# Optimization experiments

Hardware: AMD Instinct MI355X
Metric: run time of the kernel (lower is better)

The kernel has to match this reference:

```python
import jax, jax.numpy as jnp
import numpy as np

N_NODES = 6144
IN_FEATURES = 256
N_HEADS = 4
N_HIDDEN = 64  # out_features, concat=False
LEAKY_SLOPE = 0.2
NEG_INF = -9e16


def setup_inputs() -> dict:
    key = jax.random.key(0)
    k1, k2, k3, k4 = jax.random.split(key, 4)
    h = jax.random.normal(k1, (N_NODES, IN_FEATURES), dtype=jnp.float32)
    adj_mat = jax.random.randint(k2, (N_NODES, N_NODES), 0, 2, dtype=jnp.int32)
    W = jax.random.normal(k3, (IN_FEATURES, N_HEADS * N_HIDDEN), dtype=jnp.float32) * 0.06
    a = jax.random.normal(k4, (N_HEADS, 2 * N_HIDDEN, 1), dtype=jnp.float32) * 0.1
    return {"h": h, "adj_mat": adj_mat, "W": W, "a": a}


def reference(h, adj_mat, W, a):
    n_nodes = h.shape[0]
    # linear transform, dropout is identity in eval mode
    ht = (h @ W).reshape(n_nodes, N_HEADS, N_HIDDEN).transpose(1, 0, 2)  # [H, N, d]
    a_src = a[:, :N_HIDDEN, 0]   # [H, d]
    a_tgt = a[:, N_HIDDEN:, 0]   # [H, d]
    src = jnp.einsum('hnd,hd->hn', ht, a_src)  # [H, N]
    tgt = jnp.einsum('hnd,hd->hn', ht, a_tgt)  # [H, N]
    e = src[:, :, None] + tgt[:, None, :]       # [H, N, N]
    e = jnp.where(e >= 0, e, LEAKY_SLOPE * e)    # leaky relu
    e = jnp.where(adj_mat[None, :, :] > 0, e, jnp.float32(NEG_INF))
    attention = jax.nn.softmax(e, axis=-1)       # [H, N, N]
    h_prime = jnp.einsum('hij,hjd->hid', attention, ht)  # [H, N, d]
    return h_prime.mean(axis=0)                  # [N, d] (concat=False)
```

## Files before the change

kernel.cpp:

```cpp
#include <hip/hip_runtime.h>
#include <hip/hip_bf16.h>

#define N_NODES 6144
#define IN_F 256
#define N_HEADS 4
#define N_HID 64
#define JS 8
#define JLEN (N_NODES / JS)
#define NW (JLEN / 32)
#define SM_STRIDE 25
#define PACK_BLOCKS 768
#define ACC_F32 (N_HEADS * N_NODES * N_HID + N_HEADS * N_NODES)
#define ZERO_F4_PER_BLOCK 520

typedef __attribute__((ext_vector_type(4))) float floatx4;
typedef _Float16 half2_t __attribute__((ext_vector_type(2)));
typedef _Float16 half8_t __attribute__((ext_vector_type(8)));
typedef __attribute__((ext_vector_type(4))) unsigned uint4_t;
typedef short short2v __attribute__((ext_vector_type(2)));

__device__ __forceinline__ void atomAddF32(float* p, float v) {
    unsafeAtomicAdd(p, v);
}

__global__ __launch_bounds__(256) void prep_kernel(
    const float* __restrict__ h, const float* __restrict__ W,
    const float* __restrict__ a, const int* __restrict__ adj,
    short* __restrict__ htF, float* __restrict__ srcv,
    unsigned* __restrict__ tE1pk, unsigned* __restrict__ tE2pk,
    unsigned long long* __restrict__ gmask, float* __restrict__ accZero)
{
    __shared__ float As[32][34];
    __shared__ float Bs[32][68];
    __shared__ float redS[32][16];
    __shared__ float redT[32][16];
    __shared__ unsigned short eh1[32], eh2[32];

    if (blockIdx.x < PACK_BLOCKS) {
        {
            float4* z = (float4*)accZero + (size_t)blockIdx.x * ZERO_F4_PER_BLOCK;
            const float4 zv = {0.f, 0.f, 0.f, 0.f};
            for (int i = threadIdx.x; i < ZERO_F4_PER_BLOCK; i += 256) z[i] = zv;
        }
        const int lane = threadIdx.x & 63;
        const int wave = threadIdx.x >> 6;
        const int wbase = (blockIdx.x * 4 + wave) * 192;
        for (int k0 = 0; k0 < 192; k0 += 16) {
            int v[16];
            #pragma unroll
            for (int s = 0; s < 16; ++s) {
                const int widx = wbase + k0 + s;
                const int r = widx / 96, c = widx % 96;
                v[s] = adj[(size_t)r * N_NODES + c * 64 + lane];
            }
            #pragma unroll
            for (int s = 0; s < 16; ++s) {
                const unsigned long long b = __ballot(v[s] > 0);
                const int widx = wbase + k0 + s;
                const int r = widx / 96, c = widx % 96;
                const int jcp = c / 12, wl = c % 12;
                if (lane == 0)
                    gmask[((size_t)jcp * N_NODES + r) * 12 + wl] = b;
            }
        }
        return;
    }

    const int gbx = blockIdx.x - PACK_BLOCKS;
    const int head = gbx & 3;
    const int i0 = (gbx >> 2) * 32;
    const int tid = threadIdx.x;
    const int tx = tid & 15, ty = tid >> 4;

    float acc[2][4] = {};

    for (int k0 = 0; k0 < IN_F; k0 += 32) {
        __syncthreads();
        {
            const int m = tid >> 3, kq = tid & 7;
            const float4 v = *(const float4*)(h + (i0 + m) * IN_F + k0 + kq * 4);
            As[kq*4+0][m] = v.x; As[kq*4+1][m] = v.y;
            As[kq*4+2][m] = v.z; As[kq*4+3][m] = v.w;
        }
        #pragma unroll
        for (int it = 0; it < 2; ++it) {
            int l = it * 256 + tid;
            int k = l >> 4, nq = l & 15;
            *(float4*)&Bs[k][nq*4] = *(const float4*)(W + (k0 + k) * 256 + head * 64 + nq * 4);
        }
        __syncthreads();
        #pragma unroll
        for (int kk = 0; kk < 32; ++kk) {
            const float2 av = *(const float2*)&As[kk][ty*2];
            const float4 bv = *(const float4*)&Bs[kk][tx*4];
            const float aa[2] = {av.x, av.y};
            const float bb[4] = {bv.x, bv.y, bv.z, bv.w};
            #pragma unroll
            for (int r = 0; r < 2; ++r)
                #pragma unroll
                for (int c = 0; c < 4; ++c)
                    acc[r][c] = fmaf(aa[r], bb[c], acc[r][c]);
        }
    }

    #pragma unroll
    for (int r = 0; r < 2; ++r)
        #pragma unroll
        for (int c2 = 0; c2 < 4; ++c2) {
            const int d = tx * 4 + c2;
            const int j = i0 + ty * 2 + r;
            const int jt = j >> 5, q = (j >> 3) & 3, u = j & 7;
            const int c = d >> 4, n = d & 15;
            const size_t F = (((((size_t)head * 192 + jt) * 4 + c) * 16 + n) * 4 + q) * 8 + u;
            const _Float16 hv = (_Float16)acc[r][c2];
            htF[F] = *(const short*)&hv;
        }

    float as_[4], at_[4];
    #pragma unroll
    for (int c = 0; c < 4; ++c) {
        as_[c] = a[head * 128 + tx * 4 + c];
        at_[c] = a[head * 128 + 64 + tx * 4 + c];
    }
    #pragma unroll
    for (int r = 0; r < 2; ++r) {
        float ps = 0.f, pt = 0.f;
        #pragma unroll
        for (int c = 0; c < 4; ++c) {
            ps = fmaf(acc[r][c], as_[c], ps);
            pt = fmaf(acc[r][c], at_[c], pt);
        }
        redS[ty*2+r][tx] = ps;
        redT[ty*2+r][tx] = pt;
    }
    __syncthreads();
    if (tid < 64) {
        const int row = tid & 31;
        const float* src = (tid < 32) ? &redS[row][0] : &redT[row][0];
        float s = 0.f;
        #pragma unroll
        for (int x = 0; x < 16; ++x) s += src[x];
        if (tid < 32) {
            srcv[head * N_NODES + i0 + row] = s;
        } else {
            const _Float16 E1 = (_Float16)__expf(s);
            const _Float16 E2 = (_Float16)__expf(0.2f * s);
            eh1[row] = *(const unsigned short*)&E1;
            eh2[row] = *(const unsigned short*)&E2;
        }
    }
    __syncthreads();
    if (tid < 16) {
        const unsigned v1 = (unsigned)eh1[2*tid] | ((unsigned)eh1[2*tid+1] << 16);
        const unsigned v2 = (unsigned)eh2[2*tid] | ((unsigned)eh2[2*tid+1] << 16);
        tE1pk[head * (N_NODES/2) + i0/2 + tid] = v1;
        tE2pk[head * (N_NODES/2) + i0/2 + tid] = v2;
    }
}

__global__ __launch_bounds__(256, 4) void gat_main_kernel(
    const unsigned* __restrict__ gmask32, const short* __restrict__ htF,
    const float* __restrict__ srcv, const unsigned* __restrict__ tE1pk,
    const unsigned* __restrict__ tE2pk,
    float* __restrict__ accNg, float* __restrict__ accDg)
{
    __shared__ unsigned smask[32 * SM_STRIDE];

    const int bid = blockIdx.x;
    const int xcd = bid & 7;
    const int idx = bid >> 3;
    const int jc = idx / 24;
    const int rb0 = ((idx % 24) * 8 + xcd) * 32;

    const int lane = threadIdx.x;
    const int head = threadIdx.y;
    const int m = lane & 15, quad = lane >> 4;
    const int jbase = jc * JLEN;
    const int tid = head * 64 + lane;

    {
        const unsigned* g = gmask32 + ((size_t)jc * N_NODES + rb0) * 24;
        #pragma unroll
        for (int it = 0; it < 3; ++it) {
            const int f = it * 256 + tid;
            smask[(f / 24) * SM_STRIDE + (f % 24)] = g[f];
        }
    }
    __syncthreads();

    half2_t e1s[2], e2s[2];
    #pragma unroll
    for (int t = 0; t < 2; ++t) {
        const float sv = srcv[head * N_NODES + rb0 + t * 16 + m];
        const _Float16 a1 = (_Float16)__expf(sv);
        const _Float16 a2 = (_Float16)__expf(0.2f * sv);
        e1s[t] = (half2_t){a1, a1};
        e2s[t] = (half2_t){a2, a2};
    }

    const short* fb = htF + ((size_t)(head * 192 + (jbase >> 5)) * 4) * 512 + (m * 4 + quad) * 8;
    const unsigned* pe1 = tE1pk + head * (N_NODES/2) + (jbase >> 1) + quad * 4;
    const unsigned* pe2 = tE2pk + head * (N_NODES/2) + (jbase >> 1) + quad * 4;

    half8_t bones;
    #pragma unroll
    for (int u = 0; u < 8; ++u) bones[u] = (_Float16)1.0f;

    floatx4 accN[2][4];
    floatx4 accD[2];
    #pragma unroll
    for (int t = 0; t < 2; ++t) {
        accD[t] = (floatx4){0,0,0,0};
        #pragma unroll
        for (int c = 0; c < 4; ++c) accN[t][c] = (floatx4){0,0,0,0};
    }

    half8_t bn[4];
    #pragma unroll
    for (int c = 0; c < 4; ++c) bn[c] = *(const half8_t*)(fb + c * 512);
    uint4_t E1n = *(const uint4_t*)pe1;
    uint4_t E2n = *(const uint4_t*)pe2;

    for (int w = 0; w < NW; ++w) {
        half8_t bc[4];
        #pragma unroll
        for (int c = 0; c < 4; ++c) bc[c] = bn[c];
        const uint4_t E1 = E1n, E2 = E2n;

        const int wn = (w + 1 < NW) ? (w + 1) : w;
        #pragma unroll
        for (int c = 0; c < 4; ++c)
            bn[c] = *(const half8_t*)(fb + (size_t)wn * 2048 + c * 512);
        E1n = *(const uint4_t*)(pe1 + wn * 16);
        E2n = *(const uint4_t*)(pe2 + wn * 16);

        const unsigned E1a[4] = {E1.x, E1.y, E1.z, E1.w};
        const unsigned E2a[4] = {E2.x, E2.y, E2.z, E2.w};

        #pragma unroll
        for (int t = 0; t < 2; ++t) {
            const unsigned bits = (smask[(t * 16 + m) * SM_STRIDE + w] >> (quad * 8)) & 0xffu;
            const short2v tt = __builtin_bit_cast(short2v, bits * 0x10001u);
            uint4_t af_u;
            #pragma unroll
            for (int p = 0; p < 4; ++p) {
                const short2v shl = (p == 0) ? (short2v){15,14} : (p == 1) ? (short2v){13,12}
                                 : (p == 2) ? (short2v){11,10} : (short2v){9,8};
                const short2v k = (tt << shl) >> (short2v){15,15};
                const half2_t p1 = __builtin_bit_cast(half2_t, E1a[p]) * e1s[t];
                const half2_t p2 = __builtin_bit_cast(half2_t, E2a[p]) * e2s[t];
                const half2_t mx = __builtin_elementwise_max(p1, p2);
                const unsigned r = __builtin_bit_cast(unsigned, mx) & __builtin_bit_cast(unsigned, k);
                if (p == 0) af_u.x = r; else if (p == 1) af_u.y = r;
                else if (p == 2) af_u.z = r; else af_u.w = r;
            }
            const half8_t af = __builtin_bit_cast(half8_t, af_u);
            #pragma unroll
            for (int c = 0; c < 4; ++c)
                accN[t][c] = __builtin_amdgcn_mfma_f32_16x16x32_f16(af, bc[c], accN[t][c], 0, 0, 0);
            accD[t] = __builtin_amdgcn_mfma_f32_16x16x32_f16(af, bones, accD[t], 0, 0, 0);
        }
    }

    const size_t nb = (size_t)head * N_NODES;
    #pragma unroll
    for (int t = 0; t < 2; ++t) {
        #pragma unroll
        for (int r = 0; r < 4; ++r) {
            const int gi = rb0 + t * 16 + quad * 4 + r;
            if (m == 0) atomAddF32(&accDg[nb + gi], accD[t][r]);
            float* np_ = accNg + (nb + gi) * N_HID + m;
            atomAddF32(np_ + 0,  accN[t][0][r]);
            atomAddF32(np_ + 16, accN[t][1][r]);
            atomAddF32(np_ + 32, accN[t][2][r]);
            atomAddF32(np_ + 48, accN[t][3][r]);
        }
    }
}

__global__ __launch_bounds__(256) void finalize_kernel(
    const float* __restrict__ accNg, const float* __restrict__ accDg,
    float* __restrict__ out)
{
    const int idx = blockIdx.x * 256 + threadIdx.x;
    if (idx >= N_NODES * 16) return;
    const int i = idx >> 4;
    const int d4 = (idx & 15) * 4;
    float sx = 0.f, sy = 0.f, sz = 0.f, sw = 0.f;
    #pragma unroll
    for (int hh = 0; hh < N_HEADS; ++hh) {
        const float4 v = *(const float4*)(accNg + ((size_t)hh * N_NODES + i) * N_HID + d4);
        const float r = 1.0f / accDg[hh * N_NODES + i];
        sx += v.x * r; sy += v.y * r; sz += v.z * r; sw += v.w * r;
    }
    float4 o; o.x = 0.25f * sx; o.y = 0.25f * sy; o.z = 0.25f * sz; o.w = 0.25f * sw;
    *(float4*)(out + (size_t)i * N_HID + d4) = o;
}

extern "C" void kernel_launch(void* const* d_in, const int* in_sizes, int n_in,
                              void* d_out, int out_size, void* d_ws, size_t ws_size,
                              hipStream_t stream)
{
    const float* h   = (const float*)d_in[0];
    const int*   adj = (const int*)d_in[1];
    const float* W   = (const float*)d_in[2];
    const float* a   = (const float*)d_in[3];
    float* out = (float*)d_out;

    char* ws = (char*)d_ws;
    short* htF = (short*)ws;
    size_t off = (size_t)N_HEADS * N_HID * N_NODES * 2;
    float* srcv = (float*)(ws + off);        off += (size_t)N_HEADS * N_NODES * 4;
    unsigned* tE1pk = (unsigned*)(ws + off); off += (size_t)N_HEADS * (N_NODES/2) * 4;
    unsigned* tE2pk = (unsigned*)(ws + off); off += (size_t)N_HEADS * (N_NODES/2) * 4;
    unsigned long long* gmask = (unsigned long long*)(ws + off);
    off += (size_t)JS * N_NODES * 12 * 8;
    float* accN = (float*)(ws + off);        off += (size_t)N_HEADS * N_NODES * N_HID * 4;
    float* accD = (float*)(ws + off);        off += (size_t)N_HEADS * N_NODES * 4;

    prep_kernel<<<PACK_BLOCKS + (N_NODES / 32) * N_HEADS, 256, 0, stream>>>(
        h, W, a, adj, htF, srcv, tE1pk, tE2pk, gmask, accN );
    gat_main_kernel<<<1536, dim3(64, 4), 0, stream>>>(
        (const unsigned*)gmask, htF, srcv, tE1pk, tE2pk, accN, accD);
    finalize_kernel<<<(N_NODES * 16 + 255) / 256, 256, 0, stream>>>(accN, accD, out);
}
```

Baseline: 304.2 us.

## Replace atomic accumulation with per-split partial buffers reduced in finalize

The main kernel now writes per-column-split partial numerators and denominators to separate slots instead of atomically adding into shared accumulators, which also removes the zeroing pass from the prep kernel. The column split count drops from 8 to 6, the mask layout becomes row-major with a padded shared-memory stride, and the next mask word is prefetched into registers one step ahead. Prep blocks for mask packing and the projection are interleaved by block parity. Finalize now reads and sums 6 partial slots per head, which adds extra global memory traffic in exchange for removing atomic contention.

```diff
diff --git a/kernel.cpp b/kernel.cpp
--- a/kernel.cpp
+++ b/kernel.cpp
@@ -5,13 +5,11 @@
 #define IN_F 256
 #define N_HEADS 4
 #define N_HID 64
-#define JS 8
+#define JS 6
 #define JLEN (N_NODES / JS)
 #define NW (JLEN / 32)
-#define SM_STRIDE 25
+#define SMW 33
 #define PACK_BLOCKS 768
-#define ACC_F32 (N_HEADS * N_NODES * N_HID + N_HEADS * N_NODES)
-#define ZERO_F4_PER_BLOCK 520
 
 typedef __attribute__((ext_vector_type(4))) float floatx4;
 typedef _Float16 half2_t __attribute__((ext_vector_type(2)));
@@ -19,16 +17,12 @@
 typedef __attribute__((ext_vector_type(4))) unsigned uint4_t;
 typedef short short2v __attribute__((ext_vector_type(2)));
 
-__device__ __forceinline__ void atomAddF32(float* p, float v) {
-    unsafeAtomicAdd(p, v);
-}
-
 __global__ __launch_bounds__(256) void prep_kernel(
     const float* __restrict__ h, const float* __restrict__ W,
     const float* __restrict__ a, const int* __restrict__ adj,
     short* __restrict__ htF, float* __restrict__ srcv,
     unsigned* __restrict__ tE1pk, unsigned* __restrict__ tE2pk,
-    unsigned long long* __restrict__ gmask, float* __restrict__ accZero)
+    unsigned long long* __restrict__ gmask)
 {
     __shared__ float As[32][34];
     __shared__ float Bs[32][68];
@@ -36,15 +30,11 @@
     __shared__ float redT[32][16];
     __shared__ unsigned short eh1[32], eh2[32];
 
-    if (blockIdx.x < PACK_BLOCKS) {
-        {
-            float4* z = (float4*)accZero + (size_t)blockIdx.x * ZERO_F4_PER_BLOCK;
-            const float4 zv = {0.f, 0.f, 0.f, 0.f};
-            for (int i = threadIdx.x; i < ZERO_F4_PER_BLOCK; i += 256) z[i] = zv;
-        }
+    if ((blockIdx.x & 1) == 0) {
+        const int pb = blockIdx.x >> 1;
         const int lane = threadIdx.x & 63;
         const int wave = threadIdx.x >> 6;
-        const int wbase = (blockIdx.x * 4 + wave) * 192;
+        const int wbase = (pb * 4 + wave) * 192;
         for (int k0 = 0; k0 < 192; k0 += 16) {
             int v[16];
             #pragma unroll
@@ -58,15 +48,14 @@
                 const unsigned long long b = __ballot(v[s] > 0);
                 const int widx = wbase + k0 + s;
                 const int r = widx / 96, c = widx % 96;
-                const int jcp = c / 12, wl = c % 12;
                 if (lane == 0)
-                    gmask[((size_t)jcp * N_NODES + r) * 12 + wl] = b;
+                    gmask[(size_t)r * 96 + c] = b;
             }
         }
         return;
     }
 
-    const int gbx = blockIdx.x - PACK_BLOCKS;
+    const int gbx = blockIdx.x >> 1;
     const int head = gbx & 3;
     const int i0 = (gbx >> 2) * 32;
     const int tid = threadIdx.x;
@@ -162,9 +151,9 @@
     const unsigned* __restrict__ gmask32, const short* __restrict__ htF,
     const float* __restrict__ srcv, const unsigned* __restrict__ tE1pk,
     const unsigned* __restrict__ tE2pk,
-    float* __restrict__ accNg, float* __restrict__ accDg)
+    float* __restrict__ pnum, float* __restrict__ pden)
 {
-    __shared__ unsigned smask[32 * SM_STRIDE];
+    __shared__ unsigned smask[32 * SMW];
 
     const int bid = blockIdx.x;
     const int xcd = bid & 7;
@@ -179,11 +168,11 @@
     const int tid = head * 64 + lane;
 
     {
-        const unsigned* g = gmask32 + ((size_t)jc * N_NODES + rb0) * 24;
-        #pragma unroll
-        for (int it = 0; it < 3; ++it) {
+        #pragma unroll
+        for (int it = 0; it < 4; ++it) {
             const int f = it * 256 + tid;
-            smask[(f / 24) * SM_STRIDE + (f % 24)] = g[f];
+            const int r = f >> 5, w = f & 31;
+            smask[r * SMW + w] = gmask32[((size_t)(rb0 + r)) * 192 + jc * 32 + w];
         }
     }
     __syncthreads();
@@ -220,12 +209,16 @@
     for (int c = 0; c < 4; ++c) bn[c] = *(const half8_t*)(fb + c * 512);
     uint4_t E1n = *(const uint4_t*)pe1;
     uint4_t E2n = *(const uint4_t*)pe2;
+    unsigned mwn[2];
+    #pragma unroll
+    for (int t = 0; t < 2; ++t) mwn[t] = smask[(t * 16 + m) * SMW + 0];
 
     for (int w = 0; w < NW; ++w) {
         half8_t bc[4];
         #pragma unroll
         for (int c = 0; c < 4; ++c) bc[c] = bn[c];
         const uint4_t E1 = E1n, E2 = E2n;
+        const unsigned mw[2] = {mwn[0], mwn[1]};
 
         const int wn = (w + 1 < NW) ? (w + 1) : w;
         #pragma unroll
@@ -233,13 +226,15 @@
             bn[c] = *(const half8_t*)(fb + (size_t)wn * 2048 + c * 512);
         E1n = *(const uint4_t*)(pe1 + wn * 16);
         E2n = *(const uint4_t*)(pe2 + wn * 16);
+        #pragma unroll
+        for (int t = 0; t < 2; ++t) mwn[t] = smask[(t * 16 + m) * SMW + wn];
 
         const unsigned E1a[4] = {E1.x, E1.y, E1.z, E1.w};
         const unsigned E2a[4] = {E2.x, E2.y, E2.z, E2.w};
 
         #pragma unroll
         for (int t = 0; t < 2; ++t) {
-            const unsigned bits = (smask[(t * 16 + m) * SM_STRIDE + w] >> (quad * 8)) & 0xffu;
+            const unsigned bits = (mw[t] >> (quad * 8)) & 0xffu;
             const short2v tt = __builtin_bit_cast(short2v, bits * 0x10001u);
             uint4_t af_u;
             #pragma unroll
@@ -262,36 +257,47 @@
         }
     }
 
-    const size_t nb = (size_t)head * N_NODES;
+    const int slot = jc * N_HEADS + head;
     #pragma unroll
     for (int t = 0; t < 2; ++t) {
+        if (m == 0) {
+            #pragma unroll
+            for (int r = 0; r < 4; ++r)
+                pden[slot * N_NODES + rb0 + t * 16 + quad * 4 + r] = accD[t][r];
+        }
         #pragma unroll
         for (int r = 0; r < 4; ++r) {
             const int gi = rb0 + t * 16 + quad * 4 + r;
-            if (m == 0) atomAddF32(&accDg[nb + gi], accD[t][r]);
-            float* np_ = accNg + (nb + gi) * N_HID + m;
-            atomAddF32(np_ + 0,  accN[t][0][r]);
-            atomAddF32(np_ + 16, accN[t][1][r]);
-            atomAddF32(np_ + 32, accN[t][2][r]);
-            atomAddF32(np_ + 48, accN[t][3][r]);
+            float* np_ = pnum + ((size_t)slot * N_NODES + gi) * N_HID + m;
+            np_[0]  = accN[t][0][r];
+            np_[16] = accN[t][1][r];
+            np_[32] = accN[t][2][r];
+            np_[48] = accN[t][3][r];
         }
     }
 }
 
-__global__ __launch_bounds__(256) void finalize_kernel(
-    const float* __restrict__ accNg, const float* __restrict__ accDg,
+__global__ __launch_bounds__(128) void finalize_kernel(
+    const float* __restrict__ pnum, const float* __restrict__ pden,
     float* __restrict__ out)
 {
-    const int idx = blockIdx.x * 256 + threadIdx.x;
+    const int idx = blockIdx.x * 128 + threadIdx.x;
     if (idx >= N_NODES * 16) return;
     const int i = idx >> 4;
     const int d4 = (idx & 15) * 4;
     float sx = 0.f, sy = 0.f, sz = 0.f, sw = 0.f;
     #pragma unroll
     for (int hh = 0; hh < N_HEADS; ++hh) {
-        const float4 v = *(const float4*)(accNg + ((size_t)hh * N_NODES + i) * N_HID + d4);
-        const float r = 1.0f / accDg[hh * N_NODES + i];
-        sx += v.x * r; sy += v.y * r; sz += v.z * r; sw += v.w * r;
+        float nx = 0.f, ny = 0.f, nz = 0.f, nw_ = 0.f, ds = 0.f;
+        #pragma unroll
+        for (int jc = 0; jc < JS; ++jc) {
+            const int slot = jc * N_HEADS + hh;
+            const float4 v = *(const float4*)(pnum + ((size_t)slot * N_NODES + i) * N_HID + d4);
+            nx += v.x; ny += v.y; nz += v.z; nw_ += v.w;
+            ds += pden[slot * N_NODES + i];
+        }
+        const float r = 1.0f / ds;
+        sx += nx * r; sy += ny * r; sz += nz * r; sw += nw_ * r;
     }
     float4 o; o.x = 0.25f * sx; o.y = 0.25f * sy; o.z = 0.25f * sz; o.w = 0.25f * sw;
     *(float4*)(out + (size_t)i * N_HID + d4) = o;
@@ -314,13 +320,14 @@
     unsigned* tE1pk = (unsigned*)(ws + off); off += (size_t)N_HEADS * (N_NODES/2) * 4;
     unsigned* tE2pk = (unsigned*)(ws + off); off += (size_t)N_HEADS * (N_NODES/2) * 4;
     unsigned long long* gmask = (unsigned long long*)(ws + off);
-    off += (size_t)JS * N_NODES * 12 * 8;
-    float* accN = (float*)(ws + off);        off += (size_t)N_HEADS * N_NODES * N_HID * 4;
-    float* accD = (float*)(ws + off);        off += (size_t)N_HEADS * N_NODES * 4;
-
-    prep_kernel<<<PACK_BLOCKS + (N_NODES / 32) * N_HEADS, 256, 0, stream>>>(
-        h, W, a, adj, htF, srcv, tE1pk, tE2pk, gmask, accN );
-    gat_main_kernel<<<1536, dim3(64, 4), 0, stream>>>(
-        (const unsigned*)gmask, htF, srcv, tE1pk, tE2pk, accN, accD);
-    finalize_kernel<<<(N_NODES * 16 + 255) / 256, 256, 0, stream>>>(accN, accD, out);
+    off += (size_t)N_NODES * 96 * 8;
+    float* pnum = (float*)(ws + off);
+    off += (size_t)JS * N_HEADS * N_NODES * N_HID * 4;
+    float* pden = (float*)(ws + off);
+
+    prep_kernel<<<2 * PACK_BLOCKS, 256, 0, stream>>>(
+        h, W, a, adj, htF, srcv, tE1pk, tE2pk, gmask);
+    gat_main_kernel<<<JS * 192, dim3(64, 4), 0, stream>>>(
+        (const unsigned*)gmask, htF, srcv, tE1pk, tE2pk, pnum, pden);
+    finalize_kernel<<<(N_NODES * 16 + 127) / 128, 128, 0, stream>>>(pnum, pden, out);
 }
```

After: 295.7 us. -2.8%, faster.
